# Kernel tuning notes

Measured on AMD Instinct MI355X. Metric: run time of the kernel, lower is better.

The kernel has to match this reference:

```python
import jax, jax.numpy as jnp
import numpy as np

H = 128      # num_hidden
C = 384      # num_in
K = 32       # neighbors
N = 10000    # nodes
SCALE = 30.0
EPS = 1e-5

def _gelu(x):
    return jax.nn.gelu(x, approximate=False)  # torch GELU default is exact erf

def _ln(x, g, b):
    m = jnp.mean(x, axis=-1, keepdims=True)
    v = jnp.mean((x - m) ** 2, axis=-1, keepdims=True)
    return (x - m) * jax.lax.rsqrt(v + EPS) * g + b

def setup_inputs() -> dict:
    key = jax.random.key(0)
    ks = jax.random.split(key, 12)
    s = lambda fan_in: 1.0 / np.sqrt(fan_in)
    # weights stored [in, out] (transposed vs torch nn.Linear)
    return {
        "h_V": jax.random.normal(ks[0], (N, H), jnp.float32),
        "h_E": jax.random.normal(ks[1], (N, K, C), jnp.float32),
        "mask_V": jnp.ones((N,), jnp.float32),
        "mask_attend": jnp.ones((N, K), jnp.float32),
        "W1_w": jax.random.uniform(ks[2], (H + C, H), jnp.float32, -s(H + C), s(H + C)),
        "W1_b": jnp.zeros((H,), jnp.float32),
        "W2_w": jax.random.uniform(ks[3], (H, H), jnp.float32, -s(H), s(H)),
        "W2_b": jnp.zeros((H,), jnp.float32),
        "W3_w": jax.random.uniform(ks[4], (H, H), jnp.float32, -s(H), s(H)),
        "W3_b": jnp.zeros((H,), jnp.float32),
        "ln1_g": jnp.ones((H,), jnp.float32),
        "ln1_b": jnp.zeros((H,), jnp.float32),
        "Win_w": jax.random.uniform(ks[5], (H, 4 * H), jnp.float32, -s(H), s(H)),
        "Win_b": jnp.zeros((4 * H,), jnp.float32),
        "Wout_w": jax.random.uniform(ks[6], (4 * H, H), jnp.float32, -s(4 * H), s(4 * H)),
        "Wout_b": jnp.zeros((H,), jnp.float32),
        "ln2_g": jnp.ones((H,), jnp.float32),
        "ln2_b": jnp.zeros((H,), jnp.float32),
    }

def reference(h_V, h_E, mask_V, mask_attend,
              W1_w, W1_b, W2_w, W2_b, W3_w, W3_b,
              ln1_g, ln1_b, Win_w, Win_b, Wout_w, Wout_b, ln2_g, ln2_b):
    # expand node features along neighbor axis and concat with edge features
    h_V_expand = jnp.broadcast_to(h_V[:, None, :], (h_V.shape[0], h_E.shape[1], h_V.shape[1]))
    h_EV = jnp.concatenate([h_V_expand, h_E], axis=-1)          # [N, K, H+C]
    # per-edge 3-layer MLP message
    h = _gelu(h_EV @ W1_w + W1_b)                               # [N, K, H]
    h = _gelu(h @ W2_w + W2_b)
    h_message = h @ W3_w + W3_b
    h_message = mask_attend[..., None] * h_message
    dh = jnp.sum(h_message, axis=-2) / SCALE                    # [N, H]
    h_V = _ln(h_V + dh, ln1_g, ln1_b)
    # position-wise FFN
    dh = _gelu(h_V @ Win_w + Win_b) @ Wout_w + Wout_b
    h_V = _ln(h_V + dh, ln2_g, ln2_b)
    h_V = mask_V[:, None] * h_V
    return h_V
```

## Files before the change

### kernel.cpp

```cpp
#include <hip/hip_runtime.h>
#include <hip/hip_bf16.h>

#define NH 128
#define NC 384
#define NK 32

typedef __attribute__((ext_vector_type(8))) short short8v;
typedef __attribute__((ext_vector_type(4))) float f32x4;

#define MFMA16(a, b, c) __builtin_amdgcn_mfma_f32_16x16x32_bf16((a), (b), (c), 0, 0, 0)

__device__ __forceinline__ ushort f2bf(float x) {
  __hip_bfloat16 h = __float2bfloat16(x);
  ushort u;
  __builtin_memcpy(&u, &h, 2);
  return u;
}

__device__ __forceinline__ short8v ld8(const ushort* p) {
  return *reinterpret_cast<const short8v*>(p);
}
__device__ __forceinline__ void st8(ushort* p, short8v v) {
  *reinterpret_cast<short8v*>(p) = v;
}

__device__ __forceinline__ short8v pack8(float4 a, float4 b) {
  short8v v;
  v[0] = (short)f2bf(a.x); v[1] = (short)f2bf(a.y);
  v[2] = (short)f2bf(a.z); v[3] = (short)f2bf(a.w);
  v[4] = (short)f2bf(b.x); v[5] = (short)f2bf(b.y);
  v[6] = (short)f2bf(b.z); v[7] = (short)f2bf(b.w);
  return v;
}

__device__ __forceinline__ float gelu_f(float x) {
  float x2 = x * x;
  float m = __builtin_fmaf(0.07135481283f, x2, 1.595769122f);
  float e = __expf(-x * m);
  return x * __builtin_amdgcn_rcpf(1.0f + e);
}

__device__ __forceinline__ void lds_barrier() {
  asm volatile("s_waitcnt lgkmcnt(0)" ::: "memory");
  __builtin_amdgcn_sched_barrier(0);
  __builtin_amdgcn_s_barrier();
}

__global__ __launch_bounds__(256) void pack_w(
    const float* __restrict__ W1, const float* __restrict__ W2,
    const float* __restrict__ W3, const float* __restrict__ Win,
    const float* __restrict__ Wout, ushort* __restrict__ ws) {
  int id = blockIdx.x * 256 + threadIdx.x;
  if (id < 65536) {
    int t = id, k = t >> 7, c = t & 127;
    ws[(((k >> 3) << 7) + c) * 8 + (k & 7)] = f2bf(W1[t]);
  } else if (id < 81920) {
    int t = id - 65536, k = t >> 7, c = t & 127;
    ws[65536 + (((k >> 3) << 7) + c) * 8 + (k & 7)] = f2bf(W2[t]);
  } else if (id < 98304) {
    int t = id - 81920, k = t >> 7, c = t & 127;
    ws[81920 + (((k >> 3) << 7) + c) * 8 + (k & 7)] = f2bf(W3[t]);
  } else if (id < 163840) {
    int t = id - 98304, k = t >> 9, c = t & 511;
    ws[98304 + (((k >> 3) << 9) + c) * 8 + (k & 7)] = f2bf(Win[t]);
  } else {
    int t = id - 163840, k = t >> 7, c = t & 127;
    ws[163840 + (((k >> 3) << 7) + c) * 8 + (k & 7)] = f2bf(Wout[t]);
  }
}


__device__ __forceinline__ void issue_chunk(const float* __restrict__ hE,
    int p, int c, int tid, int N, float4& a, float4& b) {
  const int r = tid >> 3;
  const int cb = (tid & 7) * 8;
  const int node = r >> 5, e = r & 31;
  int n = 2 * p + node;
  if (n >= N) n = 0;
  const float* g = hE + ((size_t)n * NK + e) * NC + c * 64 + cb;
  const float4* gp = reinterpret_cast<const float4*>(g);
  a = gp[0];
  b = gp[1];
}

__device__ __forceinline__ void convert_regs(ushort* __restrict__ sC, int tid,
    float4 a, float4 b, bool zz) {
  const int r = tid >> 3, cg = tid & 7;
  short8v v = zz ? (short8v){0, 0, 0, 0, 0, 0, 0, 0} : pack8(a, b);
  st8(sC + r * 64 + ((cg ^ (r & 7)) << 3), v);
}

__device__ __forceinline__ void mfma_chunk64(const ushort* __restrict__ sC,
    const ushort* __restrict__ W1p, int j, f32x4 acc[4],
    int g, int lr, int outcol) {
#pragma unroll
  for (int jj = 0; jj < 2; ++jj) {
    short8v bfr = ld8(W1p + (((16 + j * 8 + jj * 4 + g) * 128) + outcol) * 8);
    const int akg = jj * 4 + g;
#pragma unroll
    for (int rt = 0; rt < 4; ++rt) {
      const int row = rt * 16 + lr;
      short8v af = ld8(sC + row * 64 + ((akg ^ (row & 7)) << 3));
      acc[rt] = MFMA16(af, bfr, acc[rt]);
    }
  }
}

__device__ __forceinline__ void mfma_chunk(const ushort* __restrict__ buf,
    const ushort* __restrict__ Wp, int ktBase, f32x4 acc[4],
    int g, int lr, int outcol) {
#pragma unroll
  for (int j = 0; j < 4; ++j) {
    short8v bfr = ld8(Wp + (((ktBase + j) * 4 + g) * 128 + outcol) * 8);
    const int kcg = j * 4 + g;
#pragma unroll
    for (int rt = 0; rt < 4; ++rt) {
      const int row = rt * 16 + lr;
      short8v af = ld8(buf + row * 128 + ((kcg ^ (row & 15)) << 3));
      acc[rt] = MFMA16(af, bfr, acc[rt]);
    }
  }
}

__device__ __forceinline__ void epi_store(ushort* __restrict__ buf,
    const f32x4 acc[4], const float* __restrict__ bias, int outcol, int g) {
  const float bs = bias[outcol];
#pragma unroll
  for (int rt = 0; rt < 4; ++rt)
#pragma unroll
    for (int i = 0; i < 4; ++i) {
      const int rr = rt * 16 + g * 4 + i;
      buf[rr * 128 + ((((outcol >> 3) ^ (rr & 15)) << 3) | (outcol & 7))] =
          f2bf(gelu_f(acc[rt][i] + bs));
    }
}

__global__ __launch_bounds__(512, 4) void msg3(
    const float* __restrict__ hV, const float* __restrict__ hE,
    const float* __restrict__ mAtt, const ushort* __restrict__ wsu,
    const float* __restrict__ b1, const float* __restrict__ b2,
    const float* __restrict__ b3, const float* __restrict__ g1,
    const float* __restrict__ be1, float* __restrict__ hmidf,
    ushort* __restrict__ hmidb, int N) {
  const ushort* W1p = wsu;
  const ushort* W2p = wsu + 65536;
  const ushort* W3p = wsu + 81920;

  __shared__ ushort sC[2][4096];
  __shared__ ushort sH2[8192];
  __shared__ ushort sHV[256];
  __shared__ float  sDh[256];
  __shared__ float  sRed[16];

  const int tid = threadIdx.x;
  const int w = tid >> 6, lane = tid & 63;
  const int g = lane >> 4, lr = lane & 15;
  const int outcol = (w << 4) + lr;
  const int p = blockIdx.x;
  const bool zz = (2 * p + ((tid >> 3) >> 5)) >= N;

  float4 eA, eB, oA, oB;

  issue_chunk(hE, p, 0, tid, N, eA, eB);
  issue_chunk(hE, p, 1, tid, N, oA, oB);
  if (tid < 32) {
    const int nd = tid >> 4, c8 = tid & 15;
    const int n = 2 * p + nd;
    const int ncl = n < N ? n : 0;
    const float4* hp = reinterpret_cast<const float4*>(hV + (size_t)ncl * NH + c8 * 8);
    float4 h0 = hp[0], h1 = hp[1];
    if (n >= N) { h0 = (float4){0.f, 0.f, 0.f, 0.f}; h1 = h0; }
    st8(sHV + nd * 128 + c8 * 8, pack8(h0, h1));
  }
  convert_regs(sC[0], tid, eA, eB, zz);
  lds_barrier();

  f32x4 acc[4];
#pragma unroll
  for (int rt = 0; rt < 4; ++rt) acc[rt] = (f32x4){0.f, 0.f, 0.f, 0.f};

#pragma unroll
  for (int kt = 0; kt < 4; ++kt) {
    short8v bfr = ld8(W1p + ((kt * 4 + g) * 128 + outcol) * 8);
    short8v a0 = ld8(sHV + kt * 32 + g * 8);
    short8v a1 = ld8(sHV + 128 + kt * 32 + g * 8);
    acc[0] = MFMA16(a0, bfr, acc[0]);
    acc[1] = MFMA16(a0, bfr, acc[1]);
    acc[2] = MFMA16(a1, bfr, acc[2]);
    acc[3] = MFMA16(a1, bfr, acc[3]);
  }

  issue_chunk(hE, p, 2, tid, N, eA, eB);
  mfma_chunk64(sC[0], W1p, 0, acc, g, lr, outcol);
  convert_regs(sC[1], tid, oA, oB, zz);
  lds_barrier();
  issue_chunk(hE, p, 3, tid, N, oA, oB);
  mfma_chunk64(sC[1], W1p, 1, acc, g, lr, outcol);
  convert_regs(sC[0], tid, eA, eB, zz);
  lds_barrier();
  issue_chunk(hE, p, 4, tid, N, eA, eB);
  mfma_chunk64(sC[0], W1p, 2, acc, g, lr, outcol);
  convert_regs(sC[1], tid, oA, oB, zz);
  lds_barrier();
  issue_chunk(hE, p, 5, tid, N, oA, oB);
  mfma_chunk64(sC[1], W1p, 3, acc, g, lr, outcol);
  convert_regs(sC[0], tid, eA, eB, zz);
  lds_barrier();
  mfma_chunk64(sC[0], W1p, 4, acc, g, lr, outcol);
  convert_regs(sC[1], tid, oA, oB, zz);
  lds_barrier();
  mfma_chunk64(sC[1], W1p, 5, acc, g, lr, outcol);
  __syncthreads();

  ushort* sH1 = &sC[0][0];
  epi_store(sH1, acc, b1, outcol, g);
  __syncthreads();

#pragma unroll
  for (int rt = 0; rt < 4; ++rt) acc[rt] = (f32x4){0.f, 0.f, 0.f, 0.f};
  mfma_chunk(sH1, W2p, 0, acc, g, lr, outcol);
  epi_store(sH2, acc, b2, outcol, g);
  __syncthreads();

#pragma unroll
  for (int rt = 0; rt < 4; ++rt) acc[rt] = (f32x4){0.f, 0.f, 0.f, 0.f};
  mfma_chunk(sH2, W3p, 0, acc, g, lr, outcol);
  {
    const float bias = b3[outcol];
    float ns0 = 0.f, ns1 = 0.f;
#pragma unroll
    for (int rt = 0; rt < 4; ++rt) {
      const int nd = rt >> 1;
      float s = 0.f;
#pragma unroll
      for (int i = 0; i < 4; ++i) {
        const int e2 = (rt & 1) * 16 + g * 4 + i;
        const float m =
            (2 * p + nd < N) ? mAtt[(size_t)(2 * p + nd) * NK + e2] : 0.f;
        s += (acc[rt][i] + bias) * m;
      }
      s += __shfl_xor(s, 16, 64);
      s += __shfl_xor(s, 32, 64);
      if (rt < 2) ns0 += s; else ns1 += s;
    }
    if (g == 0) { sDh[outcol] = ns0; sDh[128 + outcol] = ns1; }
  }
  __syncthreads();

  float x_ln = 0.f;
  if (tid < 256) {
    const int nd = tid >> 7, i = tid & 127;
    const int gn = 2 * p + nd;
    if (gn < N)
      x_ln = hV[(size_t)gn * NH + i] + sDh[nd * NH + i] * (1.f / 30.f);
    float s = x_ln, qv = x_ln * x_ln;
#pragma unroll
    for (int d = 1; d < 64; d <<= 1) {
      s += __shfl_xor(s, d, 64);
      qv += __shfl_xor(qv, d, 64);
    }
    if (lane == 0) { sRed[w * 2] = s; sRed[w * 2 + 1] = qv; }
  }
  __syncthreads();
  if (tid < 256) {
    const int nd = tid >> 7, i = tid & 127;
    const int gn = 2 * p + nd;
    if (gn < N) {
      const int wb = nd * 2;
      const float s = sRed[wb * 2] + sRed[wb * 2 + 2];
      const float qv = sRed[wb * 2 + 1] + sRed[wb * 2 + 3];
      const float mean = s * (1.f / 128.f);
      const float var = qv * (1.f / 128.f) - mean * mean;
      const float y = (x_ln - mean) * rsqrtf(var + 1e-5f) * g1[i] + be1[i];
      hmidf[(size_t)gn * NH + i] = y;
      hmidb[(size_t)gn * NH + i] = f2bf(y);
    }
  }
}

__global__ __launch_bounds__(512, 4) void ffn32(
    const ushort* __restrict__ wsu, const float* __restrict__ binf,
    const float* __restrict__ boutf, const float* __restrict__ g2,
    const float* __restrict__ be2, const float* __restrict__ maskV,
    const float* __restrict__ hmidf, const ushort* __restrict__ hmidb,
    float* __restrict__ out, int N) {
  const ushort* Winp = wsu + 98304;
  const ushort* Woutp = wsu + 163840;

  __shared__ ushort sX[32 * 128];
  __shared__ ushort sHf[32 * 512];
  __shared__ float  sY[32 * 132];

  const int tid = threadIdx.x;
  const int w = tid >> 6, lane = tid & 63;
  const int g = lane >> 4, lr = lane & 15;
  const int n0 = blockIdx.x * 32;

  {
    const int rr = tid >> 4, c8 = tid & 15;
    const int n = n0 + rr;
    short8v v = {0, 0, 0, 0, 0, 0, 0, 0};
    if (n < N) v = ld8(hmidb + (size_t)n * NH + c8 * 8);
    st8(sX + rr * 128 + ((c8 ^ (rr & 15)) << 3), v);
  }
  __syncthreads();

  {
    f32x4 accI[4][2];
#pragma unroll
    for (int ct = 0; ct < 4; ++ct) {
      accI[ct][0] = (f32x4){0.f, 0.f, 0.f, 0.f};
      accI[ct][1] = accI[ct][0];
    }
#pragma unroll
    for (int kt = 0; kt < 4; ++kt) {
      const int kcg = kt * 4 + g;
      short8v a0 = ld8(sX + lr * 128 + ((kcg ^ lr) << 3));
      short8v a1 = ld8(sX + (16 + lr) * 128 + ((kcg ^ lr) << 3));
#pragma unroll
      for (int ct = 0; ct < 4; ++ct) {
        const int col = (w << 6) + ct * 16 + lr;
        short8v b = ld8(Winp + (kcg * 512 + col) * 8);
        accI[ct][0] = MFMA16(a0, b, accI[ct][0]);
        accI[ct][1] = MFMA16(a1, b, accI[ct][1]);
      }
    }
#pragma unroll
    for (int ct = 0; ct < 4; ++ct) {
      const int col = (w << 6) + ct * 16 + lr;
      const float bi = binf[col];
      const int c8 = col >> 3;
#pragma unroll
      for (int rt = 0; rt < 2; ++rt)
#pragma unroll
        for (int i = 0; i < 4; ++i) {
          const int rr = rt * 16 + g * 4 + i;
          sHf[rr * 512 + (((c8 ^ (rr & 15)) << 3) | (col & 7))] =
              f2bf(gelu_f(accI[ct][rt][i] + bi));
        }
    }
  }
  __syncthreads();

  f32x4 o0 = (f32x4){0.f, 0.f, 0.f, 0.f}, o1 = o0;
  const int ocol = (w << 4) + lr;
#pragma unroll
  for (int kt = 0; kt < 16; ++kt) {
    const int kcg = kt * 4 + g;
    short8v b = ld8(Woutp + (kcg * 128 + ocol) * 8);
    short8v a0 = ld8(sHf + lr * 512 + ((kcg ^ lr) << 3));
    short8v a1 = ld8(sHf + (16 + lr) * 512 + ((kcg ^ lr) << 3));
    o0 = MFMA16(a0, b, o0);
    o1 = MFMA16(a1, b, o1);
  }
  {
    const float bo = boutf[ocol];
#pragma unroll
    for (int rt = 0; rt < 2; ++rt) {
      const f32x4 oo = rt ? o1 : o0;
#pragma unroll
      for (int i = 0; i < 4; ++i) {
        const int rr = rt * 16 + g * 4 + i;
        const int n = n0 + rr;
        const float resid = (n < N) ? hmidf[(size_t)n * NH + ocol] : 0.f;
        sY[rr * 132 + ocol] = oo[i] + bo + resid;
      }
    }
  }
  __syncthreads();

  {
    const int rr = tid >> 4, qq = tid & 15;
    const int n = n0 + rr;
    float vals[8];
    float s = 0.f, qs = 0.f;
    const float* yr = sY + rr * 132 + qq * 8;
#pragma unroll
    for (int j = 0; j < 8; ++j) { float x = yr[j]; vals[j] = x; s += x; qs += x * x; }
    s += __shfl_xor(s, 1, 64);  qs += __shfl_xor(qs, 1, 64);
    s += __shfl_xor(s, 2, 64);  qs += __shfl_xor(qs, 2, 64);
    s += __shfl_xor(s, 4, 64);  qs += __shfl_xor(qs, 4, 64);
    s += __shfl_xor(s, 8, 64);  qs += __shfl_xor(qs, 8, 64);
    const float mean = s * (1.f / 128.f);
    const float var = qs * (1.f / 128.f) - mean * mean;
    const float rs = rsqrtf(var + 1e-5f);
    if (n < N) {
      const float mv = maskV[n];
#pragma unroll
      for (int j = 0; j < 8; ++j) {
        const int col = qq * 8 + j;
        out[(size_t)n * NH + col] = ((vals[j] - mean) * rs * g2[col] + be2[col]) * mv;
      }
    }
  }
}

extern "C" void kernel_launch(void* const* d_in, const int* in_sizes, int n_in,
                              void* d_out, int out_size, void* d_ws, size_t ws_size,
                              hipStream_t stream) {
  const float* hV   = (const float*)d_in[0];
  const float* hE   = (const float*)d_in[1];
  const float* mV   = (const float*)d_in[2];
  const float* mAtt = (const float*)d_in[3];
  const float* W1   = (const float*)d_in[4];
  const float* b1   = (const float*)d_in[5];
  const float* W2   = (const float*)d_in[6];
  const float* b2   = (const float*)d_in[7];
  const float* W3   = (const float*)d_in[8];
  const float* b3   = (const float*)d_in[9];
  const float* g1   = (const float*)d_in[10];
  const float* be1  = (const float*)d_in[11];
  const float* Win  = (const float*)d_in[12];
  const float* binf = (const float*)d_in[13];
  const float* Wout = (const float*)d_in[14];
  const float* bout = (const float*)d_in[15];
  const float* g2   = (const float*)d_in[16];
  const float* be2  = (const float*)d_in[17];

  const int N = in_sizes[0] / NH;

  ushort* wsu = (ushort*)d_ws;
  float*  hmidf = (float*)((char*)d_ws + 458752);
  ushort* hmidb = (ushort*)((char*)d_ws + 458752 + (size_t)N * NH * 4);

  pack_w<<<896, 256, 0, stream>>>(W1, W2, W3, Win, Wout, wsu);

  const int pairs = (N + 1) / 2;
  msg3<<<pairs, 512, 0, stream>>>(hV, hE, mAtt, wsu, b1, b2, b3, g1, be1,
                                  hmidf, hmidb, N);
  ffn32<<<(N + 31) / 32, 512, 0, stream>>>(wsu, binf, bout, g2, be2, mV,
                                           hmidf, hmidb, (float*)d_out, N);
  (void)n_in; (void)out_size; (void)ws_size;
}
```

Before: 164.9 us.

## Process four nodes per block in message kernel instead of two

```diff
diff --git a/kernel.cpp b/kernel.cpp
--- a/kernel.cpp
+++ b/kernel.cpp
@@ -70,35 +70,43 @@
 }
 
 
-__device__ __forceinline__ void issue_chunk(const float* __restrict__ hE,
-    int p, int c, int tid, int N, float4& a, float4& b) {
-  const int r = tid >> 3;
-  const int cb = (tid & 7) * 8;
+__device__ __forceinline__ void issue_chunk4(const float* __restrict__ hE,
+    int q, int c, int tid, int N,
+    float4& a, float4& b, float4& cc, float4& d) {
+  const int r = tid >> 2;
+  const int cb = (tid & 3) * 16;
   const int node = r >> 5, e = r & 31;
-  int n = 2 * p + node;
+  int n = 4 * q + node;
   if (n >= N) n = 0;
   const float* g = hE + ((size_t)n * NK + e) * NC + c * 64 + cb;
   const float4* gp = reinterpret_cast<const float4*>(g);
-  a = gp[0];
-  b = gp[1];
-}
-
-__device__ __forceinline__ void convert_regs(ushort* __restrict__ sC, int tid,
-    float4 a, float4 b, bool zz) {
-  const int r = tid >> 3, cg = tid & 7;
-  short8v v = zz ? (short8v){0, 0, 0, 0, 0, 0, 0, 0} : pack8(a, b);
-  st8(sC + r * 64 + ((cg ^ (r & 7)) << 3), v);
-}
-
-__device__ __forceinline__ void mfma_chunk64(const ushort* __restrict__ sC,
-    const ushort* __restrict__ W1p, int j, f32x4 acc[4],
+  a = gp[0]; b = gp[1]; cc = gp[2]; d = gp[3];
+}
+
+__device__ __forceinline__ void convert_regs4(ushort* __restrict__ sC, int tid,
+    float4 a, float4 b, float4 cc, float4 d, bool zz) {
+  const int r = tid >> 2, cg0 = (tid & 3) * 2;
+  short8v v0, v1;
+  if (zz) {
+    v0 = (short8v){0, 0, 0, 0, 0, 0, 0, 0};
+    v1 = v0;
+  } else {
+    v0 = pack8(a, b);
+    v1 = pack8(cc, d);
+  }
+  st8(sC + r * 64 + ((cg0 ^ (r & 7)) << 3), v0);
+  st8(sC + r * 64 + (((cg0 + 1) ^ (r & 7)) << 3), v1);
+}
+
+__device__ __forceinline__ void mfma_chunk64_8(const ushort* __restrict__ sC,
+    const ushort* __restrict__ W1p, int j, f32x4 acc[8],
     int g, int lr, int outcol) {
 #pragma unroll
   for (int jj = 0; jj < 2; ++jj) {
     short8v bfr = ld8(W1p + (((16 + j * 8 + jj * 4 + g) * 128) + outcol) * 8);
     const int akg = jj * 4 + g;
 #pragma unroll
-    for (int rt = 0; rt < 4; ++rt) {
+    for (int rt = 0; rt < 8; ++rt) {
       const int row = rt * 16 + lr;
       short8v af = ld8(sC + row * 64 + ((akg ^ (row & 7)) << 3));
       acc[rt] = MFMA16(af, bfr, acc[rt]);
@@ -106,15 +114,14 @@
   }
 }
 
-__device__ __forceinline__ void mfma_chunk(const ushort* __restrict__ buf,
-    const ushort* __restrict__ Wp, int ktBase, f32x4 acc[4],
-    int g, int lr, int outcol) {
+__device__ __forceinline__ void mfma_chunk_8(const ushort* __restrict__ buf,
+    const ushort* __restrict__ Wp, f32x4 acc[8], int g, int lr, int outcol) {
 #pragma unroll
   for (int j = 0; j < 4; ++j) {
-    short8v bfr = ld8(Wp + (((ktBase + j) * 4 + g) * 128 + outcol) * 8);
+    short8v bfr = ld8(Wp + ((j * 4 + g) * 128 + outcol) * 8);
     const int kcg = j * 4 + g;
 #pragma unroll
-    for (int rt = 0; rt < 4; ++rt) {
+    for (int rt = 0; rt < 8; ++rt) {
       const int row = rt * 16 + lr;
       short8v af = ld8(buf + row * 128 + ((kcg ^ (row & 15)) << 3));
       acc[rt] = MFMA16(af, bfr, acc[rt]);
@@ -122,11 +129,11 @@
   }
 }
 
-__device__ __forceinline__ void epi_store(ushort* __restrict__ buf,
-    const f32x4 acc[4], const float* __restrict__ bias, int outcol, int g) {
+__device__ __forceinline__ void epi_store_8(ushort* __restrict__ buf,
+    const f32x4 acc[8], const float* __restrict__ bias, int outcol, int g) {
   const float bs = bias[outcol];
 #pragma unroll
-  for (int rt = 0; rt < 4; ++rt)
+  for (int rt = 0; rt < 8; ++rt)
 #pragma unroll
     for (int i = 0; i < 4; ++i) {
       const int rr = rt * 16 + g * 4 + i;
@@ -135,7 +142,7 @@
     }
 }
 
-__global__ __launch_bounds__(512, 4) void msg3(
+__global__ __launch_bounds__(512, 4) void msg8(
     const float* __restrict__ hV, const float* __restrict__ hE,
     const float* __restrict__ mAtt, const ushort* __restrict__ wsu,
     const float* __restrict__ b1, const float* __restrict__ b2,
@@ -146,113 +153,118 @@
   const ushort* W2p = wsu + 65536;
   const ushort* W3p = wsu + 81920;
 
-  __shared__ ushort sC[2][4096];
-  __shared__ ushort sH2[8192];
-  __shared__ ushort sHV[256];
-  __shared__ float  sDh[256];
+  __shared__ ushort sC[2][8192];
+  __shared__ ushort sH2[16384];
+  __shared__ ushort sHV[512];
+  __shared__ float  sDh[512];
   __shared__ float  sRed[16];
 
   const int tid = threadIdx.x;
   const int w = tid >> 6, lane = tid & 63;
   const int g = lane >> 4, lr = lane & 15;
   const int outcol = (w << 4) + lr;
-  const int p = blockIdx.x;
-  const bool zz = (2 * p + ((tid >> 3) >> 5)) >= N;
-
-  float4 eA, eB, oA, oB;
-
-  issue_chunk(hE, p, 0, tid, N, eA, eB);
-  issue_chunk(hE, p, 1, tid, N, oA, oB);
-  if (tid < 32) {
+  const int q = blockIdx.x;
+  const bool zz = (4 * q + (tid >> 7)) >= N;
+
+  float4 eA, eB, eC, eD, oA, oB, oC, oD;
+
+  issue_chunk4(hE, q, 0, tid, N, eA, eB, eC, eD);
+  issue_chunk4(hE, q, 1, tid, N, oA, oB, oC, oD);
+  if (tid < 64) {
     const int nd = tid >> 4, c8 = tid & 15;
-    const int n = 2 * p + nd;
+    const int n = 4 * q + nd;
     const int ncl = n < N ? n : 0;
     const float4* hp = reinterpret_cast<const float4*>(hV + (size_t)ncl * NH + c8 * 8);
     float4 h0 = hp[0], h1 = hp[1];
     if (n >= N) { h0 = (float4){0.f, 0.f, 0.f, 0.f}; h1 = h0; }
     st8(sHV + nd * 128 + c8 * 8, pack8(h0, h1));
   }
-  convert_regs(sC[0], tid, eA, eB, zz);
-  lds_barrier();
-
-  f32x4 acc[4];
-#pragma unroll
-  for (int rt = 0; rt < 4; ++rt) acc[rt] = (f32x4){0.f, 0.f, 0.f, 0.f};
+  convert_regs4(sC[0], tid, eA, eB, eC, eD, zz);
+  lds_barrier();
+
+  f32x4 acc[8];
+#pragma unroll
+  for (int rt = 0; rt < 8; ++rt) acc[rt] = (f32x4){0.f, 0.f, 0.f, 0.f};
 
 #pragma unroll
   for (int kt = 0; kt < 4; ++kt) {
     short8v bfr = ld8(W1p + ((kt * 4 + g) * 128 + outcol) * 8);
-    short8v a0 = ld8(sHV + kt * 32 + g * 8);
-    short8v a1 = ld8(sHV + 128 + kt * 32 + g * 8);
-    acc[0] = MFMA16(a0, bfr, acc[0]);
-    acc[1] = MFMA16(a0, bfr, acc[1]);
-    acc[2] = MFMA16(a1, bfr, acc[2]);
-    acc[3] = MFMA16(a1, bfr, acc[3]);
-  }
-
-  issue_chunk(hE, p, 2, tid, N, eA, eB);
-  mfma_chunk64(sC[0], W1p, 0, acc, g, lr, outcol);
-  convert_regs(sC[1], tid, oA, oB, zz);
-  lds_barrier();
-  issue_chunk(hE, p, 3, tid, N, oA, oB);
-  mfma_chunk64(sC[1], W1p, 1, acc, g, lr, outcol);
-  convert_regs(sC[0], tid, eA, eB, zz);
-  lds_barrier();
-  issue_chunk(hE, p, 4, tid, N, eA, eB);
-  mfma_chunk64(sC[0], W1p, 2, acc, g, lr, outcol);
-  convert_regs(sC[1], tid, oA, oB, zz);
-  lds_barrier();
-  issue_chunk(hE, p, 5, tid, N, oA, oB);
-  mfma_chunk64(sC[1], W1p, 3, acc, g, lr, outcol);
-  convert_regs(sC[0], tid, eA, eB, zz);
-  lds_barrier();
-  mfma_chunk64(sC[0], W1p, 4, acc, g, lr, outcol);
-  convert_regs(sC[1], tid, oA, oB, zz);
-  lds_barrier();
-  mfma_chunk64(sC[1], W1p, 5, acc, g, lr, outcol);
+#pragma unroll
+    for (int nd = 0; nd < 4; ++nd) {
+      short8v a0 = ld8(sHV + nd * 128 + kt * 32 + g * 8);
+      acc[nd * 2] = MFMA16(a0, bfr, acc[nd * 2]);
+    }
+  }
+#pragma unroll
+  for (int nd = 0; nd < 4; ++nd) acc[nd * 2 + 1] = acc[nd * 2];
+
+  issue_chunk4(hE, q, 2, tid, N, eA, eB, eC, eD);
+  mfma_chunk64_8(sC[0], W1p, 0, acc, g, lr, outcol);
+  convert_regs4(sC[1], tid, oA, oB, oC, oD, zz);
+  lds_barrier();
+  issue_chunk4(hE, q, 3, tid, N, oA, oB, oC, oD);
+  mfma_chunk64_8(sC[1], W1p, 1, acc, g, lr, outcol);
+  convert_regs4(sC[0], tid, eA, eB, eC, eD, zz);
+  lds_barrier();
+  issue_chunk4(hE, q, 4, tid, N, eA, eB, eC, eD);
+  mfma_chunk64_8(sC[0], W1p, 2, acc, g, lr, outcol);
+  convert_regs4(sC[1], tid, oA, oB, oC, oD, zz);
+  lds_barrier();
+  issue_chunk4(hE, q, 5, tid, N, oA, oB, oC, oD);
+  mfma_chunk64_8(sC[1], W1p, 3, acc, g, lr, outcol);
+  convert_regs4(sC[0], tid, eA, eB, eC, eD, zz);
+  lds_barrier();
+  mfma_chunk64_8(sC[0], W1p, 4, acc, g, lr, outcol);
+  convert_regs4(sC[1], tid, oA, oB, oC, oD, zz);
+  lds_barrier();
+  mfma_chunk64_8(sC[1], W1p, 5, acc, g, lr, outcol);
   __syncthreads();
 
   ushort* sH1 = &sC[0][0];
-  epi_store(sH1, acc, b1, outcol, g);
-  __syncthreads();
-
-#pragma unroll
-  for (int rt = 0; rt < 4; ++rt) acc[rt] = (f32x4){0.f, 0.f, 0.f, 0.f};
-  mfma_chunk(sH1, W2p, 0, acc, g, lr, outcol);
-  epi_store(sH2, acc, b2, outcol, g);
-  __syncthreads();
-
-#pragma unroll
-  for (int rt = 0; rt < 4; ++rt) acc[rt] = (f32x4){0.f, 0.f, 0.f, 0.f};
-  mfma_chunk(sH2, W3p, 0, acc, g, lr, outcol);
+  epi_store_8(sH1, acc, b1, outcol, g);
+  __syncthreads();
+
+#pragma unroll
+  for (int rt = 0; rt < 8; ++rt) acc[rt] = (f32x4){0.f, 0.f, 0.f, 0.f};
+  mfma_chunk_8(sH1, W2p, acc, g, lr, outcol);
+  epi_store_8(sH2, acc, b2, outcol, g);
+  __syncthreads();
+
+#pragma unroll
+  for (int rt = 0; rt < 8; ++rt) acc[rt] = (f32x4){0.f, 0.f, 0.f, 0.f};
+  mfma_chunk_8(sH2, W3p, acc, g, lr, outcol);
   {
     const float bias = b3[outcol];
-    float ns0 = 0.f, ns1 = 0.f;
-#pragma unroll
-    for (int rt = 0; rt < 4; ++rt) {
-      const int nd = rt >> 1;
+    float ns[4];
+#pragma unroll
+    for (int nd = 0; nd < 4; ++nd) {
       float s = 0.f;
 #pragma unroll
-      for (int i = 0; i < 4; ++i) {
-        const int e2 = (rt & 1) * 16 + g * 4 + i;
-        const float m =
-            (2 * p + nd < N) ? mAtt[(size_t)(2 * p + nd) * NK + e2] : 0.f;
-        s += (acc[rt][i] + bias) * m;
-      }
+      for (int half = 0; half < 2; ++half)
+#pragma unroll
+        for (int i = 0; i < 4; ++i) {
+          const int e2 = half * 16 + g * 4 + i;
+          const float m =
+              (4 * q + nd < N) ? mAtt[(size_t)(4 * q + nd) * NK + e2] : 0.f;
+          s += (acc[nd * 2 + half][i] + bias) * m;
+        }
       s += __shfl_xor(s, 16, 64);
       s += __shfl_xor(s, 32, 64);
-      if (rt < 2) ns0 += s; else ns1 += s;
-    }
-    if (g == 0) { sDh[outcol] = ns0; sDh[128 + outcol] = ns1; }
+      ns[nd] = s;
+    }
+    if (g == 0) {
+#pragma unroll
+      for (int nd = 0; nd < 4; ++nd) sDh[nd * 128 + outcol] = ns[nd];
+    }
   }
   __syncthreads();
 
   float x_ln = 0.f;
-  if (tid < 256) {
+  {
     const int nd = tid >> 7, i = tid & 127;
-    const int gn = 2 * p + nd;
+    const int gn = 4 * q + nd;
     if (gn < N)
-      x_ln = hV[(size_t)gn * NH + i] + sDh[nd * NH + i] * (1.f / 30.f);
+      x_ln = hV[(size_t)gn * NH + i] + sDh[nd * 128 + i] * (1.f / 30.f);
     float s = x_ln, qv = x_ln * x_ln;
 #pragma unroll
     for (int d = 1; d < 64; d <<= 1) {
@@ -262,13 +274,12 @@
     if (lane == 0) { sRed[w * 2] = s; sRed[w * 2 + 1] = qv; }
   }
   __syncthreads();
-  if (tid < 256) {
+  {
     const int nd = tid >> 7, i = tid & 127;
-    const int gn = 2 * p + nd;
+    const int gn = 4 * q + nd;
     if (gn < N) {
-      const int wb = nd * 2;
-      const float s = sRed[wb * 2] + sRed[wb * 2 + 2];
-      const float qv = sRed[wb * 2 + 1] + sRed[wb * 2 + 3];
+      const float s = sRed[nd * 4] + sRed[nd * 4 + 2];
+      const float qv = sRed[nd * 4 + 1] + sRed[nd * 4 + 3];
       const float mean = s * (1.f / 128.f);
       const float var = qv * (1.f / 128.f) - mean * mean;
       const float y = (x_ln - mean) * rsqrtf(var + 1e-5f) * g1[i] + be1[i];
@@ -425,8 +436,8 @@
 
   pack_w<<<896, 256, 0, stream>>>(W1, W2, W3, Win, Wout, wsu);
 
-  const int pairs = (N + 1) / 2;
-  msg3<<<pairs, 512, 0, stream>>>(hV, hE, mAtt, wsu, b1, b2, b3, g1, be1,
+  const int quads = (N + 3) / 4;
+  msg8<<<quads, 512, 0, stream>>>(hV, hE, mAtt, wsu, b1, b2, b3, g1, be1,
                                   hmidf, hmidb, N);
   ffn32<<<(N + 31) / 32, 512, 0, stream>>>(wsu, binf, bout, g2, be2, mV,
                                            hmidf, hmidb, (float*)d_out, N);
```

New measurement: 161.9 us, median of 2. Within noise of the previous version (-1.8%).
